# Performance work log

Hardware: AMD Instinct MI355X
Metric: run time of the kernel (lower is better)

## Reference

```python
import jax, jax.numpy as jnp
import numpy as np

N_NODES = 100000
N_EDGES = 800000
N_GRAPHS = 2000
IN_DIM = 64
HID = 32
HEADS = 4
NEG_SLOPE = 0.2


def _glorot(key, shape, fan_in, fan_out):
    lim = np.sqrt(6.0 / (fan_in + fan_out)).astype(np.float32)
    return jax.random.uniform(key, shape, jnp.float32, -lim, lim)


def setup_inputs() -> dict:
    key = jax.random.key(0)
    ks = jax.random.split(key, 16)
    x = jax.random.normal(ks[0], (N_NODES, IN_DIM), jnp.float32)
    edge_index = jax.random.randint(ks[1], (2, N_EDGES), 0, N_NODES, jnp.int64)
    batch = jnp.sort(jax.random.randint(ks[2], (N_NODES,), 0, N_GRAPHS, jnp.int64))
    HF = HEADS * HID
    params = {
        "W1": _glorot(ks[3], (IN_DIM, HF), IN_DIM, HF),
        "a1_src": _glorot(ks[4], (HEADS, HID), HID, HID),
        "a1_dst": _glorot(ks[5], (HEADS, HID), HID, HID),
        "b1": jnp.zeros((HF,), jnp.float32),
        "W2": _glorot(ks[6], (HF, HF), HF, HF),
        "a2_src": _glorot(ks[7], (HEADS, HID), HID, HID),
        "a2_dst": _glorot(ks[8], (HEADS, HID), HID, HID),
        "b2": jnp.zeros((HF,), jnp.float32),
        "W3": _glorot(ks[9], (HF, HF), HF, HF),
        "a3_src": _glorot(ks[10], (HEADS, HID), HID, HID),
        "a3_dst": _glorot(ks[11], (HEADS, HID), HID, HID),
        "b3": jnp.zeros((HID,), jnp.float32),  # concat=False -> bias over out dim
        "Wm1": _glorot(ks[12], (HID, 64), HID, 64),
        "bm1": jnp.zeros((64,), jnp.float32),
        "Wm2": _glorot(ks[13], (64, 1), 64, 1),
        "bm2": jnp.zeros((1,), jnp.float32),
    }
    return {"x": x, "edge_index": edge_index, "batch": batch, **params}


def gat_conv(x, src, dst, W, a_src, a_dst, bias, concat):
    # PyG GATConv (eval mode, self-loops already in src/dst).
    N = x.shape[0]
    H, F = a_src.shape
    h = (x @ W).reshape(N, H, F)                     # [N,H,F]
    as_n = jnp.sum(h * a_src, axis=-1)               # [N,H] per-node src term
    ad_n = jnp.sum(h * a_dst, axis=-1)               # [N,H] per-node dst term
    logits = jax.nn.leaky_relu(as_n[src] + ad_n[dst], NEG_SLOPE)  # [Et,H]
    # segment softmax over incoming edges of each dst node
    m = jax.ops.segment_max(logits, dst, num_segments=N)          # [N,H]
    e = jnp.exp(logits - m[dst])
    denom = jax.ops.segment_sum(e, dst, num_segments=N)           # [N,H], >0 via self-loops
    alpha = e / denom[dst]                                        # [Et,H]
    msg = h[src] * alpha[:, :, None]                              # [Et,H,F]
    out = jax.ops.segment_sum(msg, dst, num_segments=N)           # [N,H,F]
    out = out.reshape(N, H * F) if concat else out.mean(axis=1)
    return out + bias


def reference(x, edge_index, batch, W1, a1_src, a1_dst, b1, W2, a2_src, a2_dst, b2,
              W3, a3_src, a3_dst, b3, Wm1, bm1, Wm2, bm2):
    N = x.shape[0]
    loops = jnp.arange(N, dtype=edge_index.dtype)
    src = jnp.concatenate([edge_index[0], loops])
    dst = jnp.concatenate([edge_index[1], loops])

    h = jax.nn.elu(gat_conv(x, src, dst, W1, a1_src, a1_dst, b1, True))
    h = jax.nn.elu(gat_conv(h, src, dst, W2, a2_src, a2_dst, b2, True))
    h = jax.nn.elu(gat_conv(h, src, dst, W3, a3_src, a3_dst, b3, False))

    # global_mean_pool over batch ids
    sums = jax.ops.segment_sum(h, batch, num_segments=N_GRAPHS)           # [G,HID]
    cnts = jax.ops.segment_sum(jnp.ones((N,), h.dtype), batch, num_segments=N_GRAPHS)
    pooled = sums / jnp.maximum(cnts, 1.0)[:, None]

    z = jax.nn.relu(pooled @ Wm1 + bm1)
    out = (z @ Wm2 + bm2).squeeze(-1)                                     # [G]
    return out
```

## Files before the change

kernel.cpp:

```cpp
#include <hip/hip_runtime.h>

#define N_NODES  100000
#define N_EDGES  800000
#define ET       900000
#define N_GRAPHS 2000
#define IN_DIM   64
#define HID      32
#define HEADS    4
#define HF       128
#define NEG_SLOPE 0.2f

typedef __attribute__((ext_vector_type(8))) short bf16x8;
typedef __attribute__((ext_vector_type(4))) float f32x4;

__device__ __forceinline__ float lrelu(float x) { return x > 0.f ? x : NEG_SLOPE * x; }
__device__ __forceinline__ float elu_f(float x) { return x > 0.f ? x : expm1f(x); }
__device__ __forceinline__ unsigned fenc(float f) {
  unsigned u = __float_as_uint(f);
  return (u & 0x80000000u) ? ~u : (u | 0x80000000u);
}
__device__ __forceinline__ float fdec(unsigned e) {
  return __uint_as_float((e & 0x80000000u) ? (e ^ 0x80000000u) : ~e);
}
__device__ __forceinline__ unsigned short bf16_rne(float f) {
  unsigned u = __float_as_uint(f);
  unsigned r = (u + 0x7fffu + ((u >> 16) & 1u)) >> 16;
  return (unsigned short)r;
}

__global__ void k_count(const int* __restrict__ ei, int* __restrict__ deg) {
  int e = blockIdx.x * 256 + threadIdx.x;
  if (e >= ET) return;
  int d = (e < N_EDGES) ? ei[N_EDGES + e] : (e - N_EDGES);
  atomicAdd(&deg[d], 1);
}

__global__ void k_scan1(const int* __restrict__ deg, int* __restrict__ rs, int* __restrict__ bsums) {
  __shared__ int sd[256];
  int t = threadIdx.x;
  int i = blockIdx.x * 256 + t;
  int v = (i < N_NODES) ? deg[i] : 0;
  sd[t] = v; __syncthreads();
  for (int s = 1; s < 256; s <<= 1) {
    int tmp = (t >= s) ? sd[t - s] : 0; __syncthreads();
    sd[t] += tmp; __syncthreads();
  }
  if (i < N_NODES) rs[i] = sd[t] - v;
  if (t == 255) bsums[blockIdx.x] = sd[255];
}

__global__ void k_scan2(int* __restrict__ bsums, int nb) {
  __shared__ int sd[512];
  int t = threadIdx.x;
  int v = (t < nb) ? bsums[t] : 0;
  sd[t] = v; __syncthreads();
  for (int s = 1; s < 512; s <<= 1) {
    int tmp = (t >= s) ? sd[t - s] : 0; __syncthreads();
    sd[t] += tmp; __syncthreads();
  }
  if (t < nb) bsums[t] = sd[t] - v;
}

__global__ void k_scan3(int* __restrict__ rs, const int* __restrict__ bsums) {
  int i = blockIdx.x * 256 + threadIdx.x;
  if (i < N_NODES) rs[i] += bsums[blockIdx.x];
  if (i == 0) rs[N_NODES] = ET;
}

__global__ void k_fill(const int* __restrict__ ei, const int* __restrict__ rs,
                       int* __restrict__ fill, int* __restrict__ csr_src) {
  int e = blockIdx.x * 256 + threadIdx.x;
  if (e >= ET) return;
  int s, d;
  if (e < N_EDGES) { s = ei[e]; d = ei[N_EDGES + e]; }
  else             { s = e - N_EDGES; d = s; }
  int pos = atomicAdd(&fill[d], 1);
  csr_src[rs[d] + pos] = s;
}

template<int K>
__global__ void k_prep(const float* __restrict__ W, const float* __restrict__ as_,
                       const float* __restrict__ ad_,
                       unsigned short* __restrict__ Bh, unsigned short* __restrict__ Bl) {
  int idx = blockIdx.x * 256 + threadIdx.x;
  if (idx >= K * 144) return;
  int k = idx / 144, c = idx % 144;
  float v = 0.f;
  if (c < 128) {
    v = W[k * 128 + c];
  } else if (c < 136) {
    int h = (c - 128) & 3;
    const float* av = (c < 132) ? as_ : ad_;
    float s = 0.f;
    for (int f = 0; f < HID; ++f) s += W[k * 128 + h * HID + f] * av[h * HID + f];
    v = s;
  }
  unsigned short hi = bf16_rne(v);
  float hf = __uint_as_float((unsigned)hi << 16);
  unsigned short lo = bf16_rne(v - hf);
  size_t dst = ((size_t)(k >> 3) * 144 + c) * 8 + (k & 7);
  Bh[dst] = hi;
  Bl[dst] = lo;
}

template<int K>
__global__ void __launch_bounds__(256, 4) k_gemm_attn(
    const float* __restrict__ X,
    const unsigned short* __restrict__ Bh, const unsigned short* __restrict__ Bl,
    float* __restrict__ H, float* __restrict__ AS, float* __restrict__ AD,
    unsigned* __restrict__ M4) {
  constexpr unsigned BB = K * 144 * 2;
  constexpr unsigned FB = 128 * 128 * 4 + 128 * 8 * 4;
  constexpr unsigned SM = (2 * BB > FB) ? 2 * BB : FB;
  __shared__ __align__(16) char smem[SM];
  short* sBh = (short*)smem;
  short* sBl = (short*)(smem + BB);
  const int t = threadIdx.x;
  const int l = t & 63;
  const int w = t >> 6;
  const int m = l & 15;
  const int g = l >> 4;
  const int row0 = blockIdx.x * 128 + w * 32;
  const int row_a = row0 + m;
  const int row_b = row0 + 16 + m;

  for (int i = t; i < K * 18; i += 256) {
    ((bf16x8*)sBh)[i] = ((const bf16x8*)Bh)[i];
    ((bf16x8*)sBl)[i] = ((const bf16x8*)Bl)[i];
  }
  __syncthreads();

  f32x4 acc[2][9];
#pragma unroll
  for (int a = 0; a < 2; ++a)
#pragma unroll
    for (int b = 0; b < 9; ++b) acc[a][b] = (f32x4){0.f, 0.f, 0.f, 0.f};

  float4 pxa0, pxb0, pxa1, pxb1;
#define LOADA(kb)                                                              \
  {                                                                            \
    pxa0 = pxb0 = pxa1 = pxb1 = make_float4(0.f, 0.f, 0.f, 0.f);               \
    if (row_a < N_NODES) {                                                     \
      const float4* xp = (const float4*)&X[(size_t)row_a * K + (kb) + g * 8];  \
      pxa0 = xp[0]; pxb0 = xp[1];                                              \
    }                                                                          \
    if (row_b < N_NODES) {                                                     \
      const float4* xp = (const float4*)&X[(size_t)row_b * K + (kb) + g * 8];  \
      pxa1 = xp[0]; pxb1 = xp[1];                                              \
    }                                                                          \
  }

  LOADA(0);
  for (int kb = 0; kb < K; kb += 32) {
    bf16x8 ahi[2], alo[2];
    {
      float xv0[8] = {pxa0.x, pxa0.y, pxa0.z, pxa0.w, pxb0.x, pxb0.y, pxb0.z, pxb0.w};
      float xv1[8] = {pxa1.x, pxa1.y, pxa1.z, pxa1.w, pxb1.x, pxb1.y, pxb1.z, pxb1.w};
#pragma unroll
      for (int j = 0; j < 8; ++j) {
        unsigned short h0 = bf16_rne(xv0[j]);
        ahi[0][j] = (short)h0;
        alo[0][j] = (short)bf16_rne(xv0[j] - __uint_as_float((unsigned)h0 << 16));
        unsigned short h1 = bf16_rne(xv1[j]);
        ahi[1][j] = (short)h1;
        alo[1][j] = (short)bf16_rne(xv1[j] - __uint_as_float((unsigned)h1 << 16));
      }
    }
    if (kb + 32 < K) LOADA(kb + 32);

    const int kfl = ((kb >> 3) + g) * 144;
#pragma unroll
    for (int tc = 0; tc < 9; ++tc) {
      bf16x8 bh = *(const bf16x8*)(sBh + (kfl + tc * 16 + m) * 8);
      bf16x8 bl = *(const bf16x8*)(sBl + (kfl + tc * 16 + m) * 8);
#pragma unroll
      for (int tr = 0; tr < 2; ++tr) {
        acc[tr][tc] = __builtin_amdgcn_mfma_f32_16x16x32_bf16(ahi[tr], bh, acc[tr][tc], 0, 0, 0);
        acc[tr][tc] = __builtin_amdgcn_mfma_f32_16x16x32_bf16(ahi[tr], bl, acc[tr][tc], 0, 0, 0);
        acc[tr][tc] = __builtin_amdgcn_mfma_f32_16x16x32_bf16(alo[tr], bh, acc[tr][tc], 0, 0, 0);
      }
    }
  }
#undef LOADA

  float vmax = -3.4e38f;
#pragma unroll
  for (int tr = 0; tr < 2; ++tr)
#pragma unroll
    for (int e = 0; e < 4; ++e) vmax = fmaxf(vmax, acc[tr][8][e]);
  vmax = fmaxf(vmax, __shfl_xor(vmax, 16));
  vmax = fmaxf(vmax, __shfl_xor(vmax, 32));
  if (g == 0 && m < 4) atomicMax(&M4[m], fenc(vmax));

  __syncthreads();
  float* sF  = (float*)smem;
  float* sAS = sF + 128 * 128;
  float* sAD = sAS + 128 * 4;
  const int wrow0 = w * 32;
#pragma unroll
  for (int tr = 0; tr < 2; ++tr) {
    int rl = wrow0 + tr * 16 + g * 4;
#pragma unroll
    for (int tc = 0; tc < 8; ++tc) {
      int col = tc * 16 + m;
#pragma unroll
      for (int e = 0; e < 4; ++e) sF[(rl + e) * 128 + col] = acc[tr][tc][e];
    }
#pragma unroll
    for (int e = 0; e < 4; ++e) {
      float v = acc[tr][8][e];
      if (m < 4) sAS[(rl + e) * 4 + m] = v;
      else if (m < 8) sAD[(rl + e) * 4 + (m - 4)] = v;
    }
  }
  __syncthreads();
  const int base = blockIdx.x * 128;
  for (int i = t; i < 128 * 32; i += 256) {
    int r = i >> 5, c4 = (i & 31) << 2;
    int gr = base + r;
    if (gr < N_NODES)
      *(float4*)&H[(size_t)gr * HF + c4] = *(const float4*)&sF[r * 128 + c4];
  }
  {
    int r = t & 127, gr = base + r;
    if (gr < N_NODES) {
      if (t < 128) *(float4*)&AS[(size_t)gr * 4] = *(const float4*)&sAS[r * 4];
      else         *(float4*)&AD[(size_t)gr * 4] = *(const float4*)&sAD[r * 4];
    }
  }
}

template<bool CONCAT>
__global__ void __launch_bounds__(256) k_aggregate(
    const int* __restrict__ rs, const int* __restrict__ csr_src,
    const float* __restrict__ H, const float* __restrict__ AS,
    const float* __restrict__ AD, const unsigned* __restrict__ M4,
    const float* __restrict__ bias, float* __restrict__ OUT) {
  int n = blockIdx.x * 8 + (threadIdx.x >> 5);
  if (n >= N_NODES) return;
  int sl = threadIdx.x & 31;
  int c = sl * 4;
  int head = sl >> 3;
  int b = rs[n], e = rs[n + 1];

  float ad = AD[4 * n + head];
  float m = lrelu(fdec(M4[head]) + ad);

  float ax = 0.f, ay = 0.f, az = 0.f, aw = 0.f, den = 0.f;
  int jj = b;
  for (; jj + 3 < e; jj += 4) {
    int s0 = csr_src[jj];
    int s1 = csr_src[jj + 1];
    int s2 = csr_src[jj + 2];
    int s3 = csr_src[jj + 3];
    float e0 = __expf(lrelu(AS[4 * s0 + head] + ad) - m);
    float e1 = __expf(lrelu(AS[4 * s1 + head] + ad) - m);
    float e2 = __expf(lrelu(AS[4 * s2 + head] + ad) - m);
    float e3 = __expf(lrelu(AS[4 * s3 + head] + ad) - m);
    float4 h0 = *(const float4*)&H[(size_t)s0 * HF + c];
    float4 h1 = *(const float4*)&H[(size_t)s1 * HF + c];
    float4 h2 = *(const float4*)&H[(size_t)s2 * HF + c];
    float4 h3 = *(const float4*)&H[(size_t)s3 * HF + c];
    ax += h0.x * e0 + h1.x * e1 + h2.x * e2 + h3.x * e3;
    ay += h0.y * e0 + h1.y * e1 + h2.y * e2 + h3.y * e3;
    az += h0.z * e0 + h1.z * e1 + h2.z * e2 + h3.z * e3;
    aw += h0.w * e0 + h1.w * e1 + h2.w * e2 + h3.w * e3;
    den += (e0 + e1) + (e2 + e3);
  }
  for (; jj < e; ++jj) {
    int s0 = csr_src[jj];
    float e0 = __expf(lrelu(AS[4 * s0 + head] + ad) - m);
    float4 h0 = *(const float4*)&H[(size_t)s0 * HF + c];
    ax += h0.x * e0; ay += h0.y * e0; az += h0.z * e0; aw += h0.w * e0;
    den += e0;
  }

  float invd = 1.f / den;
  if (CONCAT) {
    float4 o;
    o.x = elu_f(ax * invd + bias[c]);
    o.y = elu_f(ay * invd + bias[c + 1]);
    o.z = elu_f(az * invd + bias[c + 2]);
    o.w = elu_f(aw * invd + bias[c + 3]);
    *(float4*)&OUT[(size_t)n * HF + c] = o;
  } else {
    ax *= invd; ay *= invd; az *= invd; aw *= invd;
    ax += __shfl_xor(ax, 8);  ay += __shfl_xor(ay, 8);
    az += __shfl_xor(az, 8);  aw += __shfl_xor(aw, 8);
    ax += __shfl_xor(ax, 16); ay += __shfl_xor(ay, 16);
    az += __shfl_xor(az, 16); aw += __shfl_xor(aw, 16);
    if (sl < 8) {
      int cc = sl * 4;
      float4 o;
      o.x = elu_f(0.25f * ax + bias[cc]);
      o.y = elu_f(0.25f * ay + bias[cc + 1]);
      o.z = elu_f(0.25f * az + bias[cc + 2]);
      o.w = elu_f(0.25f * aw + bias[cc + 3]);
      *(float4*)&OUT[(size_t)n * HID + cc] = o;
    }
  }
}

__global__ void __launch_bounds__(64) k_pool_mlp(
    const int* __restrict__ batch, const float* __restrict__ H3,
    const float* __restrict__ Wm1, const float* __restrict__ bm1,
    const float* __restrict__ Wm2, const float* __restrict__ bm2,
    float* __restrict__ OUT) {
  int g = blockIdx.x;
  int t = threadIdx.x;
  __shared__ float pooled[HID];
  int lo = 0, hi = N_NODES;
  while (lo < hi) { int mid = (lo + hi) >> 1; if (batch[mid] < g) lo = mid + 1; else hi = mid; }
  int start = lo;
  hi = N_NODES;
  while (lo < hi) { int mid = (lo + hi) >> 1; if (batch[mid] < g + 1) lo = mid + 1; else hi = mid; }
  int end = lo;
  if (t < HID) {
    float s = 0.f;
    for (int n = start; n < end; ++n) s += H3[(size_t)n * HID + t];
    float cnt = (float)(end - start);
    pooled[t] = s / fmaxf(cnt, 1.f);
  }
  __syncthreads();
  float z = bm1[t];
#pragma unroll
  for (int f = 0; f < HID; ++f) z += pooled[f] * Wm1[f * 64 + t];
  z = fmaxf(z, 0.f);
  float p = z * Wm2[t];
  for (int off = 32; off > 0; off >>= 1) p += __shfl_down(p, off);
  if (t == 0) OUT[g] = p + bm2[0];
}

extern "C" void kernel_launch(void* const* d_in, const int* in_sizes, int n_in,
                              void* d_out, int out_size, void* d_ws, size_t ws_size,
                              hipStream_t stream) {
  const float* x    = (const float*)d_in[0];
  const int*   ei   = (const int*)d_in[1];
  const int*   batch= (const int*)d_in[2];
  const float* W1   = (const float*)d_in[3];
  const float* a1s  = (const float*)d_in[4];
  const float* a1d  = (const float*)d_in[5];
  const float* b1   = (const float*)d_in[6];
  const float* W2   = (const float*)d_in[7];
  const float* a2s  = (const float*)d_in[8];
  const float* a2d  = (const float*)d_in[9];
  const float* b2   = (const float*)d_in[10];
  const float* W3   = (const float*)d_in[11];
  const float* a3s  = (const float*)d_in[12];
  const float* a3d  = (const float*)d_in[13];
  const float* b3   = (const float*)d_in[14];
  const float* Wm1  = (const float*)d_in[15];
  const float* bm1  = (const float*)d_in[16];
  const float* Wm2  = (const float*)d_in[17];
  const float* bm2  = (const float*)d_in[18];
  float* out = (float*)d_out;

  char* p = (char*)d_ws;
  auto take = [&](size_t bytes) { char* r = p; p += (bytes + 255) & ~(size_t)255; return r; };
  float*          bufA = (float*)take((size_t)N_NODES * HF * 4);
  float*          bufB = (float*)take((size_t)N_NODES * HF * 4);
  float*          AS   = (float*)take((size_t)N_NODES * HEADS * 4);
  float*          AD   = (float*)take((size_t)N_NODES * HEADS * 4);
  unsigned*       M4   = (unsigned*)take(3 * 4 * 4);
  int*            deg  = (int*)take((size_t)N_NODES * 4);
  int*            rs   = (int*)take((size_t)(N_NODES + 1) * 4);
  int*            csr  = (int*)take((size_t)ET * 4);
  int*            bsums= (int*)take((size_t)512 * 4);
  unsigned short* Wh1  = (unsigned short*)take((size_t)IN_DIM * 144 * 2);
  unsigned short* Wl1  = (unsigned short*)take((size_t)IN_DIM * 144 * 2);
  unsigned short* Wh2  = (unsigned short*)take((size_t)HF * 144 * 2);
  unsigned short* Wl2  = (unsigned short*)take((size_t)HF * 144 * 2);
  unsigned short* Wh3  = (unsigned short*)take((size_t)HF * 144 * 2);
  unsigned short* Wl3  = (unsigned short*)take((size_t)HF * 144 * 2);

  unsigned* M4a = M4;
  unsigned* M4b = M4 + 4;
  unsigned* M4c = M4 + 8;

  const int nb_scan = (N_NODES + 255) / 256;

  k_prep<IN_DIM><<<(IN_DIM * 144 + 255) / 256, 256, 0, stream>>>(W1, a1s, a1d, Wh1, Wl1);
  k_prep<HF><<<(HF * 144 + 255) / 256, 256, 0, stream>>>(W2, a2s, a2d, Wh2, Wl2);
  k_prep<HF><<<(HF * 144 + 255) / 256, 256, 0, stream>>>(W3, a3s, a3d, Wh3, Wl3);

  hipMemsetAsync(deg, 0, (size_t)N_NODES * 4, stream);
  hipMemsetAsync(M4, 0, 48, stream);
  k_count<<<(ET + 255) / 256, 256, 0, stream>>>(ei, deg);
  k_scan1<<<nb_scan, 256, 0, stream>>>(deg, rs, bsums);
  k_scan2<<<1, 512, 0, stream>>>(bsums, nb_scan);
  k_scan3<<<nb_scan, 256, 0, stream>>>(rs, bsums);
  hipMemsetAsync(deg, 0, (size_t)N_NODES * 4, stream);
  k_fill<<<(ET + 255) / 256, 256, 0, stream>>>(ei, rs, deg, csr);

  const int gb = (N_NODES + 127) / 128;
  const int ab = (N_NODES + 7) / 8;

  k_gemm_attn<IN_DIM><<<gb, 256, 0, stream>>>(x, Wh1, Wl1, bufA, AS, AD, M4a);
  k_aggregate<true><<<ab, 256, 0, stream>>>(rs, csr, bufA, AS, AD, M4a, b1, bufB);
  k_gemm_attn<HF><<<gb, 256, 0, stream>>>(bufB, Wh2, Wl2, bufA, AS, AD, M4b);
  k_aggregate<true><<<ab, 256, 0, stream>>>(rs, csr, bufA, AS, AD, M4b, b2, bufB);
  k_gemm_attn<HF><<<gb, 256, 0, stream>>>(bufB, Wh3, Wl3, bufA, AS, AD, M4c);
  k_aggregate<false><<<ab, 256, 0, stream>>>(rs, csr, bufA, AS, AD, M4c, b3, bufB);
  k_pool_mlp<<<N_GRAPHS, 64, 0, stream>>>(batch, bufB, Wm1, bm1, Wm2, bm2, out);
}
```

Before: 518.5 us.

## Shrink GEMM shared memory by staging B in K-halves and epilogue in two passes

```diff
diff --git a/kernel.cpp b/kernel.cpp
--- a/kernel.cpp
+++ b/kernel.cpp
@@ -109,12 +109,10 @@
     const unsigned short* __restrict__ Bh, const unsigned short* __restrict__ Bl,
     float* __restrict__ H, float* __restrict__ AS, float* __restrict__ AD,
     unsigned* __restrict__ M4) {
-  constexpr unsigned BB = K * 144 * 2;
-  constexpr unsigned FB = 128 * 128 * 4 + 128 * 8 * 4;
-  constexpr unsigned SM = (2 * BB > FB) ? 2 * BB : FB;
-  __shared__ __align__(16) char smem[SM];
+  constexpr int KH = 64;
+  __shared__ __align__(16) char smem[2 * KH * 144 * 2];
   short* sBh = (short*)smem;
-  short* sBl = (short*)(smem + BB);
+  short* sBl = (short*)(smem + KH * 144 * 2);
   const int t = threadIdx.x;
   const int l = t & 63;
   const int w = t >> 6;
@@ -123,12 +121,6 @@
   const int row0 = blockIdx.x * 128 + w * 32;
   const int row_a = row0 + m;
   const int row_b = row0 + 16 + m;
-
-  for (int i = t; i < K * 18; i += 256) {
-    ((bf16x8*)sBh)[i] = ((const bf16x8*)Bh)[i];
-    ((bf16x8*)sBl)[i] = ((const bf16x8*)Bl)[i];
-  }
-  __syncthreads();
 
   f32x4 acc[2][9];
 #pragma unroll
@@ -151,33 +143,43 @@
   }
 
   LOADA(0);
-  for (int kb = 0; kb < K; kb += 32) {
-    bf16x8 ahi[2], alo[2];
-    {
-      float xv0[8] = {pxa0.x, pxa0.y, pxa0.z, pxa0.w, pxb0.x, pxb0.y, pxb0.z, pxb0.w};
-      float xv1[8] = {pxa1.x, pxa1.y, pxa1.z, pxa1.w, pxb1.x, pxb1.y, pxb1.z, pxb1.w};
-#pragma unroll
-      for (int j = 0; j < 8; ++j) {
-        unsigned short h0 = bf16_rne(xv0[j]);
-        ahi[0][j] = (short)h0;
-        alo[0][j] = (short)bf16_rne(xv0[j] - __uint_as_float((unsigned)h0 << 16));
-        unsigned short h1 = bf16_rne(xv1[j]);
-        ahi[1][j] = (short)h1;
-        alo[1][j] = (short)bf16_rne(xv1[j] - __uint_as_float((unsigned)h1 << 16));
+  for (int h = 0; h < K / KH; ++h) {
+    __syncthreads();
+    for (int i = t; i < KH * 18; i += 256) {
+      ((bf16x8*)sBh)[i] = ((const bf16x8*)Bh)[h * (KH * 18) + i];
+      ((bf16x8*)sBl)[i] = ((const bf16x8*)Bl)[h * (KH * 18) + i];
+    }
+    __syncthreads();
+#pragma unroll
+    for (int cc = 0; cc < 2; ++cc) {
+      int kb = h * KH + cc * 32;
+      bf16x8 ahi[2], alo[2];
+      {
+        float xv0[8] = {pxa0.x, pxa0.y, pxa0.z, pxa0.w, pxb0.x, pxb0.y, pxb0.z, pxb0.w};
+        float xv1[8] = {pxa1.x, pxa1.y, pxa1.z, pxa1.w, pxb1.x, pxb1.y, pxb1.z, pxb1.w};
+#pragma unroll
+        for (int j = 0; j < 8; ++j) {
+          unsigned short h0 = bf16_rne(xv0[j]);
+          ahi[0][j] = (short)h0;
+          alo[0][j] = (short)bf16_rne(xv0[j] - __uint_as_float((unsigned)h0 << 16));
+          unsigned short h1 = bf16_rne(xv1[j]);
+          ahi[1][j] = (short)h1;
+          alo[1][j] = (short)bf16_rne(xv1[j] - __uint_as_float((unsigned)h1 << 16));
+        }
       }
-    }
-    if (kb + 32 < K) LOADA(kb + 32);
-
-    const int kfl = ((kb >> 3) + g) * 144;
-#pragma unroll
-    for (int tc = 0; tc < 9; ++tc) {
-      bf16x8 bh = *(const bf16x8*)(sBh + (kfl + tc * 16 + m) * 8);
-      bf16x8 bl = *(const bf16x8*)(sBl + (kfl + tc * 16 + m) * 8);
-#pragma unroll
-      for (int tr = 0; tr < 2; ++tr) {
-        acc[tr][tc] = __builtin_amdgcn_mfma_f32_16x16x32_bf16(ahi[tr], bh, acc[tr][tc], 0, 0, 0);
-        acc[tr][tc] = __builtin_amdgcn_mfma_f32_16x16x32_bf16(ahi[tr], bl, acc[tr][tc], 0, 0, 0);
-        acc[tr][tc] = __builtin_amdgcn_mfma_f32_16x16x32_bf16(alo[tr], bh, acc[tr][tc], 0, 0, 0);
+      if (kb + 32 < K) LOADA(kb + 32);
+
+      const int kfl = (cc * 4 + g) * 144;
+#pragma unroll
+      for (int tc = 0; tc < 9; ++tc) {
+        bf16x8 bh = *(const bf16x8*)(sBh + (kfl + tc * 16 + m) * 8);
+        bf16x8 bl = *(const bf16x8*)(sBl + (kfl + tc * 16 + m) * 8);
+#pragma unroll
+        for (int tr = 0; tr < 2; ++tr) {
+          acc[tr][tc] = __builtin_amdgcn_mfma_f32_16x16x32_bf16(ahi[tr], bh, acc[tr][tc], 0, 0, 0);
+          acc[tr][tc] = __builtin_amdgcn_mfma_f32_16x16x32_bf16(ahi[tr], bl, acc[tr][tc], 0, 0, 0);
+          acc[tr][tc] = __builtin_amdgcn_mfma_f32_16x16x32_bf16(alo[tr], bh, acc[tr][tc], 0, 0, 0);
+        }
       }
     }
   }
@@ -192,40 +194,45 @@
   vmax = fmaxf(vmax, __shfl_xor(vmax, 32));
   if (g == 0 && m < 4) atomicMax(&M4[m], fenc(vmax));
 
-  __syncthreads();
   float* sF  = (float*)smem;
-  float* sAS = sF + 128 * 128;
-  float* sAD = sAS + 128 * 4;
-  const int wrow0 = w * 32;
-#pragma unroll
-  for (int tr = 0; tr < 2; ++tr) {
-    int rl = wrow0 + tr * 16 + g * 4;
-#pragma unroll
-    for (int tc = 0; tc < 8; ++tc) {
-      int col = tc * 16 + m;
-#pragma unroll
-      for (int e = 0; e < 4; ++e) sF[(rl + e) * 128 + col] = acc[tr][tc][e];
-    }
-#pragma unroll
-    for (int e = 0; e < 4; ++e) {
-      float v = acc[tr][8][e];
-      if (m < 4) sAS[(rl + e) * 4 + m] = v;
-      else if (m < 8) sAD[(rl + e) * 4 + (m - 4)] = v;
-    }
-  }
-  __syncthreads();
-  const int base = blockIdx.x * 128;
-  for (int i = t; i < 128 * 32; i += 256) {
-    int r = i >> 5, c4 = (i & 31) << 2;
-    int gr = base + r;
-    if (gr < N_NODES)
-      *(float4*)&H[(size_t)gr * HF + c4] = *(const float4*)&sF[r * 128 + c4];
-  }
-  {
-    int r = t & 127, gr = base + r;
-    if (gr < N_NODES) {
-      if (t < 128) *(float4*)&AS[(size_t)gr * 4] = *(const float4*)&sAS[r * 4];
-      else         *(float4*)&AD[(size_t)gr * 4] = *(const float4*)&sAD[r * 4];
+  float* sAS = sF + 64 * 128;
+  float* sAD = sAS + 64 * 4;
+#pragma unroll
+  for (int pass = 0; pass < 2; ++pass) {
+    __syncthreads();
+    if ((w >> 1) == pass) {
+      int rl0 = (w & 1) * 32;
+#pragma unroll
+      for (int tr = 0; tr < 2; ++tr) {
+        int rl = rl0 + tr * 16 + g * 4;
+#pragma unroll
+        for (int tc = 0; tc < 8; ++tc) {
+          int col = tc * 16 + m;
+#pragma unroll
+          for (int e = 0; e < 4; ++e) sF[(rl + e) * 128 + col] = acc[tr][tc][e];
+        }
+#pragma unroll
+        for (int e = 0; e < 4; ++e) {
+          float v = acc[tr][8][e];
+          if (m < 4) sAS[(rl + e) * 4 + m] = v;
+          else if (m < 8) sAD[(rl + e) * 4 + (m - 4)] = v;
+        }
+      }
+    }
+    __syncthreads();
+    const int base = blockIdx.x * 128 + pass * 64;
+    for (int i = t; i < 64 * 32; i += 256) {
+      int r = i >> 5, c4 = (i & 31) << 2;
+      int gr = base + r;
+      if (gr < N_NODES)
+        *(float4*)&H[(size_t)gr * HF + c4] = *(const float4*)&sF[r * 128 + c4];
+    }
+    if (t < 64) {
+      int gr = base + t;
+      if (gr < N_NODES) *(float4*)&AS[(size_t)gr * 4] = *(const float4*)&sAS[t * 4];
+    } else if (t < 128) {
+      int gr = base + (t - 64);
+      if (gr < N_NODES) *(float4*)&AD[(size_t)gr * 4] = *(const float4*)&sAD[(t - 64) * 4];
     }
   }
 }
```

New measurement: 538.8 us. +3.9%, slower.
